# Kernel optimization log

Measured on AMD Instinct MI355X. Metric: run time of the kernel, lower is better.

The kernel has to match this reference:

```python
import jax, jax.numpy as jnp
import numpy as np
from functools import partial

N_QUBIT = 20
K = 1
PAULI_STRINGS = ['IX', 'IY', 'IZ', 'XI', 'XX', 'XY', 'XZ', 'YI', 'YX', 'YY', 'YZ', 'ZI', 'ZX', 'ZY', 'ZZ']

_C = np.float32(np.cos(np.pi / 4))  # = sin(pi/4)
# RY(-pi/2) = [[cos(-pi/4), -sin(-pi/4)], [sin(-pi/4), cos(-pi/4)]]
RY_NEG90 = np.array([[_C, _C], [-_C, _C]], dtype=np.complex64)
# RX(+pi/2) = [[cos(pi/4), -i sin(pi/4)], [-i sin(pi/4), cos(pi/4)]]
RX_POS90 = np.array([[_C, -1j * _C], [-1j * _C, _C]], dtype=np.complex64)


def _rx(t):
    h = t.astype(jnp.complex64) * 0.5
    c, s = jnp.cos(h), jnp.sin(h)
    i = jnp.complex64(1j)
    return jnp.stack([jnp.stack([c, -i * s]), jnp.stack([-i * s, c])])


def _ry(t):
    h = t.astype(jnp.complex64) * 0.5
    c, s = jnp.cos(h), jnp.sin(h)
    return jnp.stack([jnp.stack([c, -s]), jnp.stack([s, c])])


def _rz(t):
    h = t.astype(jnp.complex64) * 0.5
    z = jnp.zeros((), jnp.complex64)
    return jnp.stack([jnp.stack([jnp.exp(-1j * h), z]), jnp.stack([z, jnp.exp(1j * h)])])


def _apply_1q(psi, U, w):
    # psi: flat (2^n,) complex64; apply 2x2 U on wire w (big-endian, wire 0 = MSB)
    psi = psi.reshape(1 << w, 2, -1)
    return jnp.einsum('ab,xby->xay', U, psi).reshape(-1)


def _apply_cnot(psi, q):
    # CNOT with control q, target q+1 (adjacent wires)
    psi = psi.reshape(1 << q, 2, 2, -1)
    return jnp.stack([psi[:, 0], psi[:, 1, ::-1]], axis=1).reshape(-1)


def _two_local(psi, theta, ps, q):
    wires = (q, q + 1)
    if 'I' in ps:
        for p, w in zip(ps, wires):
            if p == 'X':
                psi = _apply_1q(psi, _rx(theta), w)
            elif p == 'Y':
                psi = _apply_1q(psi, _ry(theta), w)
            elif p == 'Z':
                psi = _apply_1q(psi, _rz(theta), w)
    else:
        for p, w in zip(ps, wires):
            if p == 'X':
                psi = _apply_1q(psi, RY_NEG90, w)
            elif p == 'Y':
                psi = _apply_1q(psi, RX_POS90, w)
        psi = _apply_cnot(psi, q)
        psi = _apply_1q(psi, _rz(theta), q + 1)
        psi = _apply_cnot(psi, q)
        for p, w in zip(ps, wires):
            if p == 'X':
                psi = _apply_1q(psi, RY_NEG90, w)
            elif p == 'Y':
                psi = _apply_1q(psi, RX_POS90, w)
    return psi


def _q_block(psi, thetas15, q):
    for i, ps in enumerate(PAULI_STRINGS):
        psi = _two_local(psi, thetas15[i], ps, q)
    return psi


def _circuit(params):
    psi = jnp.zeros(1 << N_QUBIT, jnp.complex64).at[0].set(1.0)
    for layer in range(K):
        for q in range(N_QUBIT - 1):
            # NB: faithful to the source, theta index is i (0..14), NOT q*15+i
            psi = jax.checkpoint(partial(_q_block, q=q))(psi, params[layer, :15])
    return jnp.abs(psi) ** 2


def setup_inputs() -> dict:
    key = jax.random.key(0)
    params = jax.random.normal(key, (K, (N_QUBIT - 1) * 15), dtype=jnp.float32) * np.float32(np.pi / 8)
    return {"params": params}


def reference(params):
    return _circuit(params)
```

## Files before the change

### kernel.cpp

```cpp
#include <hip/hip_runtime.h>

typedef float2 cpx;

__device__ __forceinline__ cpx cmul(cpx a, cpx b){
  return make_float2(a.x*b.x - a.y*b.y, a.x*b.y + a.y*b.x);
}
__device__ __forceinline__ cpx cadd(cpx a, cpx b){ return make_float2(a.x+b.x, a.y+b.y); }
__device__ __forceinline__ cpx czero(){ return make_float2(0.f,0.f); }

__device__ __forceinline__ cpx basis_e(int p, int i, int j){
  const float C = 0.70710678f;
  if (p==1){ float s = (i==1 && j==0) ? -C : C; return make_float2(s, 0.f); }
  else if (p==2){ if (i==j) return make_float2(C,0.f); return make_float2(0.f,-C); }
  else { return make_float2(i==j ? 1.f : 0.f, 0.f); }
}

__device__ __forceinline__ cpx rot_e(int p, int i, int j, float ch, float sh){
  if (p==1){ if (i==j) return make_float2(ch,0.f); return make_float2(0.f,-sh); }
  else if (p==2){ if (i==j) return make_float2(ch,0.f); return make_float2(i==1?sh:-sh, 0.f); }
  else { if (i!=j) return czero(); return make_float2(ch, i==0?-sh:sh); }
}

__device__ __forceinline__ cpx gate_entry(int i, int r, int c, float ch, float sh){
  int pa = i>>2, pb = i&3;
  if (pa==0 || pb==0){
    int p = pa ? pa : pb;
    if (pa) return ((r&1)==(c&1))   ? rot_e(p, r>>1, c>>1, ch, sh) : czero();
    else    return ((r>>1)==(c>>1)) ? rot_e(p, r&1,  c&1,  ch, sh) : czero();
  } else {
    cpx em = make_float2(ch,-sh), ep = make_float2(ch,sh);
    cpx s = czero();
    #pragma unroll
    for (int m=0;m<4;m++){
      cpx Prm = cmul(basis_e(pa, r>>1, m>>1), basis_e(pb, r&1, m&1));
      cpx Pmc = cmul(basis_e(pa, m>>1, c>>1), basis_e(pb, m&1, c&1));
      cpx d = (m==0 || m==3) ? em : ep;
      s = cadd(s, cmul(cmul(Prm, d), Pmc));
    }
    return s;
  }
}

#define SELT(bb, m00,m01,m10,m11) \
  m00 = (bb) ? t100 : t000; m01 = (bb) ? t101 : t001; \
  m10 = (bb) ? t110 : t010; m11 = (bb) ? t111 : t011;

__global__ __launch_bounds__(256) void mps_fused(const float* __restrict__ params,
                                                 float* __restrict__ out){
  __shared__ cpx Gm[16][16];
  __shared__ cpx P[8][16];
  __shared__ cpx Q[4][16];
  __shared__ cpx Tl[8];
  __shared__ cpx u4[16][2];
  __shared__ cpx M4p[16][5];
  __shared__ cpx f4p[16][3];
  const int t = threadIdx.x;

  if (t >= 16){
    int i = t>>4, e = t&15;
    float h = 0.5f*params[i-1];
    Gm[i][e] = gate_entry(i, e>>2, e&3, __cosf(h), __sinf(h));
  }
  __syncthreads();

  if (t < 128){
    int p = t>>4, e = t&15, r = e>>2, c = e&3;
    if (p < 7){
      cpx s = czero();
      #pragma unroll
      for (int k=0;k<4;k++) s = cadd(s, cmul(Gm[2*p+2][r*4+k], Gm[2*p+1][k*4+c]));
      P[p][e] = s;
    } else {
      P[7][e] = Gm[15][e];
    }
  }
  __syncthreads();

  if (t < 64){
    int p = t>>4, e = t&15, r = e>>2, c = e&3;
    cpx s = czero();
    #pragma unroll
    for (int k=0;k<4;k++) s = cadd(s, cmul(P[2*p+1][r*4+k], P[2*p][k*4+c]));
    Q[p][e] = s;
  }
  __syncthreads();

  if (t < 8){
    int z=(t>>2)&1, yi=(t>>1)&1, yo=t&1;
    int a=(z<<1)|yo, b=yi<<1;
    cpx r0=Q[3][a*4+0], r1=Q[3][a*4+1], r2=Q[3][a*4+2], r3=Q[3][a*4+3];
    cpx n0,n1,n2,n3;
    n0 = cadd(cadd(cmul(r0,Q[2][0]), cmul(r1,Q[2][4])), cadd(cmul(r2,Q[2][8]),  cmul(r3,Q[2][12])));
    n1 = cadd(cadd(cmul(r0,Q[2][1]), cmul(r1,Q[2][5])), cadd(cmul(r2,Q[2][9]),  cmul(r3,Q[2][13])));
    n2 = cadd(cadd(cmul(r0,Q[2][2]), cmul(r1,Q[2][6])), cadd(cmul(r2,Q[2][10]), cmul(r3,Q[2][14])));
    n3 = cadd(cadd(cmul(r0,Q[2][3]), cmul(r1,Q[2][7])), cadd(cmul(r2,Q[2][11]), cmul(r3,Q[2][15])));
    r0=n0; r1=n1; r2=n2; r3=n3;
    n0 = cadd(cadd(cmul(r0,Q[1][0]), cmul(r1,Q[1][4])), cadd(cmul(r2,Q[1][8]),  cmul(r3,Q[1][12])));
    n1 = cadd(cadd(cmul(r0,Q[1][1]), cmul(r1,Q[1][5])), cadd(cmul(r2,Q[1][9]),  cmul(r3,Q[1][13])));
    n2 = cadd(cadd(cmul(r0,Q[1][2]), cmul(r1,Q[1][6])), cadd(cmul(r2,Q[1][10]), cmul(r3,Q[1][14])));
    n3 = cadd(cadd(cmul(r0,Q[1][3]), cmul(r1,Q[1][7])), cadd(cmul(r2,Q[1][11]), cmul(r3,Q[1][15])));
    r0=n0; r1=n1; r2=n2; r3=n3;
    cpx s = cadd(cadd(cmul(r0,Q[0][b]), cmul(r1,Q[0][4+b])), cadd(cmul(r2,Q[0][8+b]), cmul(r3,Q[0][12+b])));
    Tl[t] = s;
  }
  __syncthreads();

  if (t < 48){
    cpx t000=Tl[0], t001=Tl[1], t010=Tl[2], t011=Tl[3];
    cpx t100=Tl[4], t101=Tl[5], t110=Tl[6], t111=Tl[7];
    int kind = t>>4, pat = t&15;
    int q3=pat>>3, q2=(pat>>2)&1, q1=(pat>>1)&1, q0=pat&1;
    cpx m00,m01,m10,m11;
    if (kind == 0){
      cpx r0 = q3 ? t100 : t000;
      cpx r1 = q3 ? t101 : t001;
      SELT(q2, m00,m01,m10,m11);
      { cpx n0 = cadd(cmul(r0,m00),cmul(r1,m10)); cpx n1 = cadd(cmul(r0,m01),cmul(r1,m11)); r0=n0; r1=n1; }
      SELT(q1, m00,m01,m10,m11);
      { cpx n0 = cadd(cmul(r0,m00),cmul(r1,m10)); cpx n1 = cadd(cmul(r0,m01),cmul(r1,m11)); r0=n0; r1=n1; }
      SELT(q0, m00,m01,m10,m11);
      { cpx n0 = cadd(cmul(r0,m00),cmul(r1,m10)); cpx n1 = cadd(cmul(r0,m01),cmul(r1,m11)); r0=n0; r1=n1; }
      u4[pat][0]=r0; u4[pat][1]=r1;
    } else if (kind == 1){
      cpx M00,M01,M10,M11;
      SELT(q3, M00,M01,M10,M11);
      SELT(q2, m00,m01,m10,m11);
      { cpx N00=cadd(cmul(M00,m00),cmul(M01,m10)), N01=cadd(cmul(M00,m01),cmul(M01,m11));
        cpx N10=cadd(cmul(M10,m00),cmul(M11,m10)), N11=cadd(cmul(M10,m01),cmul(M11,m11));
        M00=N00; M01=N01; M10=N10; M11=N11; }
      SELT(q1, m00,m01,m10,m11);
      { cpx N00=cadd(cmul(M00,m00),cmul(M01,m10)), N01=cadd(cmul(M00,m01),cmul(M01,m11));
        cpx N10=cadd(cmul(M10,m00),cmul(M11,m10)), N11=cadd(cmul(M10,m01),cmul(M11,m11));
        M00=N00; M01=N01; M10=N10; M11=N11; }
      SELT(q0, m00,m01,m10,m11);
      { cpx N00=cadd(cmul(M00,m00),cmul(M01,m10)), N01=cadd(cmul(M00,m01),cmul(M01,m11));
        cpx N10=cadd(cmul(M10,m00),cmul(M11,m10)), N11=cadd(cmul(M10,m01),cmul(M11,m11));
        M00=N00; M01=N01; M10=N10; M11=N11; }
      M4p[pat][0]=M00; M4p[pat][1]=M01; M4p[pat][2]=M10; M4p[pat][3]=M11;
    } else {
      cpx v0 = q1 ? (q0 ? t101 : t100) : (q0 ? t001 : t000);
      cpx v1 = q1 ? (q0 ? t111 : t110) : (q0 ? t011 : t010);
      SELT(q2, m00,m01,m10,m11);
      { cpx n0 = cadd(cmul(m00,v0),cmul(m01,v1)); cpx n1 = cadd(cmul(m10,v0),cmul(m11,v1)); v0=n0; v1=n1; }
      SELT(q3, m00,m01,m10,m11);
      { cpx n0 = cadd(cmul(m00,v0),cmul(m01,v1)); cpx n1 = cadd(cmul(m10,v0),cmul(m11,v1)); v0=n0; v1=n1; }
      f4p[pat][0]=v0; f4p[pat][1]=v1;
    }
  }
  __syncthreads();

  unsigned bid = blockIdx.x;
  cpx r0 = u4[bid>>6][0], r1 = u4[bid>>6][1];
  {
    const cpx* Ma = M4p[(bid>>2)&15u];
    cpx n0 = cadd(cmul(r0,Ma[0]), cmul(r1,Ma[2]));
    cpx n1 = cadd(cmul(r0,Ma[1]), cmul(r1,Ma[3]));
    r0=n0; r1=n1;
  }
  {
    const cpx* Mb = M4p[((bid&3u)<<2)|((unsigned)(t>>6)&3u)];
    cpx n0 = cadd(cmul(r0,Mb[0]), cmul(r1,Mb[2]));
    cpx n1 = cadd(cmul(r0,Mb[1]), cmul(r1,Mb[3]));
    r0=n0; r1=n1;
  }
  {
    const cpx* Mc = M4p[(t>>2)&15];
    cpx n0 = cadd(cmul(r0,Mc[0]), cmul(r1,Mc[2]));
    cpx n1 = cadd(cmul(r0,Mc[1]), cmul(r1,Mc[3]));
    r0=n0; r1=n1;
  }
  int fb = (t&3)<<2;
  float4 res; cpx y;
  y = cadd(cmul(r0, f4p[fb  ][0]), cmul(r1, f4p[fb  ][1])); res.x = y.x*y.x + y.y*y.y;
  y = cadd(cmul(r0, f4p[fb|1][0]), cmul(r1, f4p[fb|1][1])); res.y = y.x*y.x + y.y*y.y;
  y = cadd(cmul(r0, f4p[fb|2][0]), cmul(r1, f4p[fb|2][1])); res.z = y.x*y.x + y.y*y.y;
  y = cadd(cmul(r0, f4p[fb|3][0]), cmul(r1, f4p[fb|3][1])); res.w = y.x*y.x + y.y*y.y;
  ((float4*)out)[(bid<<8) | (unsigned)t] = res;
}

extern "C" void kernel_launch(void* const* d_in, const int* in_sizes, int n_in,
                              void* d_out, int out_size, void* d_ws, size_t ws_size,
                              hipStream_t stream) {
  const float* params = (const float*)d_in[0];
  mps_fused<<<1024, 256, 0, stream>>>(params, (float*)d_out);
}
```

Baseline: 11.57 us.

## Run gate-product tree in one wavefront with wave barriers and closed-form gates

Moves the 4x4 gate-matrix product reduction (P, Q, new R level, Tl) and the transfer-matrix setup into a single 64-thread wavefront, replacing block-wide __syncthreads with wave-level barriers plus an LDS waitcnt. Adds a tree-reduction level so the serial chain of matrix products in the Tl stage becomes one short product. Also replaces the basis-sum construction of the two-qubit Pauli rotation gate with a closed form cos*P + i*sin*diag entry. The aim is to shorten the serial prologue that every block repeats before writing its outputs. It relies on the LDS accesses being ordered within the wave by the wave barrier and waitcnt.

```diff
diff --git a/kernel.cpp b/kernel.cpp
--- a/kernel.cpp
+++ b/kernel.cpp
@@ -8,17 +8,17 @@
 __device__ __forceinline__ cpx cadd(cpx a, cpx b){ return make_float2(a.x+b.x, a.y+b.y); }
 __device__ __forceinline__ cpx czero(){ return make_float2(0.f,0.f); }
 
-__device__ __forceinline__ cpx basis_e(int p, int i, int j){
-  const float C = 0.70710678f;
-  if (p==1){ float s = (i==1 && j==0) ? -C : C; return make_float2(s, 0.f); }
-  else if (p==2){ if (i==j) return make_float2(C,0.f); return make_float2(0.f,-C); }
-  else { return make_float2(i==j ? 1.f : 0.f, 0.f); }
-}
-
 __device__ __forceinline__ cpx rot_e(int p, int i, int j, float ch, float sh){
   if (p==1){ if (i==j) return make_float2(ch,0.f); return make_float2(0.f,-sh); }
   else if (p==2){ if (i==j) return make_float2(ch,0.f); return make_float2(i==1?sh:-sh, 0.f); }
   else { if (i!=j) return czero(); return make_float2(ch, i==0?-sh:sh); }
+}
+
+__device__ __forceinline__ cpx Ae(int p, int i, int j){
+  if (p==3) return make_float2(i==j?1.f:0.f, 0.f);
+  if (i==j) return czero();
+  if (p==1) return make_float2(i==0?1.f:-1.f, 0.f);
+  return make_float2(0.f,-1.f);
 }
 
 __device__ __forceinline__ cpx gate_entry(int i, int r, int c, float ch, float sh){
@@ -27,19 +27,16 @@
     int p = pa ? pa : pb;
     if (pa) return ((r&1)==(c&1))   ? rot_e(p, r>>1, c>>1, ch, sh) : czero();
     else    return ((r>>1)==(c>>1)) ? rot_e(p, r&1,  c&1,  ch, sh) : czero();
-  } else {
-    cpx em = make_float2(ch,-sh), ep = make_float2(ch,sh);
-    cpx s = czero();
-    #pragma unroll
-    for (int m=0;m<4;m++){
-      cpx Prm = cmul(basis_e(pa, r>>1, m>>1), basis_e(pb, r&1, m&1));
-      cpx Pmc = cmul(basis_e(pa, m>>1, c>>1), basis_e(pb, m&1, c&1));
-      cpx d = (m==0 || m==3) ? em : ep;
-      s = cadd(s, cmul(cmul(Prm, d), Pmc));
-    }
-    return s;
   }
+  cpx a = cmul(Ae(pa, r>>1, c>>1), Ae(pb, r&1, c&1));
+  cpx g = make_float2(ch*a.x, ch*a.y);
+  if (r==c){ float zz = (r==0 || r==3) ? 1.f : -1.f; g.y -= sh*zz; }
+  return g;
 }
+
+#define WSYNC() do { __builtin_amdgcn_wave_barrier(); \
+  asm volatile("s_waitcnt lgkmcnt(0)" ::: "memory"); \
+  __builtin_amdgcn_wave_barrier(); } while(0)
 
 #define SELT(bb, m00,m01,m10,m11) \
   m00 = (bb) ? t100 : t000; m01 = (bb) ? t101 : t001; \
@@ -50,6 +47,7 @@
   __shared__ cpx Gm[16][16];
   __shared__ cpx P[8][16];
   __shared__ cpx Q[4][16];
+  __shared__ cpx R[2][16];
   __shared__ cpx Tl[8];
   __shared__ cpx u4[16][2];
   __shared__ cpx M4p[16][5];
@@ -63,88 +61,91 @@
   }
   __syncthreads();
 
-  if (t < 128){
-    int p = t>>4, e = t&15, r = e>>2, c = e&3;
-    if (p < 7){
+  if (t < 64){
+    #pragma unroll
+    for (int jj=0; jj<2; ++jj){
+      int j = t + jj*64;
+      int p = j>>4, e = j&15, r = e>>2, c = e&3;
+      if (p < 7){
+        cpx s = czero();
+        #pragma unroll
+        for (int k=0;k<4;k++) s = cadd(s, cmul(Gm[2*p+2][r*4+k], Gm[2*p+1][k*4+c]));
+        P[p][e] = s;
+      } else {
+        P[7][e] = Gm[15][e];
+      }
+    }
+    WSYNC();
+
+    {
+      int p = t>>4, e = t&15, r = e>>2, c = e&3;
       cpx s = czero();
       #pragma unroll
-      for (int k=0;k<4;k++) s = cadd(s, cmul(Gm[2*p+2][r*4+k], Gm[2*p+1][k*4+c]));
-      P[p][e] = s;
-    } else {
-      P[7][e] = Gm[15][e];
+      for (int k=0;k<4;k++) s = cadd(s, cmul(P[2*p+1][r*4+k], P[2*p][k*4+c]));
+      Q[p][e] = s;
     }
-  }
-  __syncthreads();
+    WSYNC();
 
-  if (t < 64){
-    int p = t>>4, e = t&15, r = e>>2, c = e&3;
-    cpx s = czero();
-    #pragma unroll
-    for (int k=0;k<4;k++) s = cadd(s, cmul(P[2*p+1][r*4+k], P[2*p][k*4+c]));
-    Q[p][e] = s;
-  }
-  __syncthreads();
+    if (t < 32){
+      int p = t>>4, e = t&15, r = e>>2, c = e&3;
+      cpx s = czero();
+      #pragma unroll
+      for (int k=0;k<4;k++) s = cadd(s, cmul(Q[2*p+1][r*4+k], Q[2*p][k*4+c]));
+      R[p][e] = s;
+    }
+    WSYNC();
 
-  if (t < 8){
-    int z=(t>>2)&1, yi=(t>>1)&1, yo=t&1;
-    int a=(z<<1)|yo, b=yi<<1;
-    cpx r0=Q[3][a*4+0], r1=Q[3][a*4+1], r2=Q[3][a*4+2], r3=Q[3][a*4+3];
-    cpx n0,n1,n2,n3;
-    n0 = cadd(cadd(cmul(r0,Q[2][0]), cmul(r1,Q[2][4])), cadd(cmul(r2,Q[2][8]),  cmul(r3,Q[2][12])));
-    n1 = cadd(cadd(cmul(r0,Q[2][1]), cmul(r1,Q[2][5])), cadd(cmul(r2,Q[2][9]),  cmul(r3,Q[2][13])));
-    n2 = cadd(cadd(cmul(r0,Q[2][2]), cmul(r1,Q[2][6])), cadd(cmul(r2,Q[2][10]), cmul(r3,Q[2][14])));
-    n3 = cadd(cadd(cmul(r0,Q[2][3]), cmul(r1,Q[2][7])), cadd(cmul(r2,Q[2][11]), cmul(r3,Q[2][15])));
-    r0=n0; r1=n1; r2=n2; r3=n3;
-    n0 = cadd(cadd(cmul(r0,Q[1][0]), cmul(r1,Q[1][4])), cadd(cmul(r2,Q[1][8]),  cmul(r3,Q[1][12])));
-    n1 = cadd(cadd(cmul(r0,Q[1][1]), cmul(r1,Q[1][5])), cadd(cmul(r2,Q[1][9]),  cmul(r3,Q[1][13])));
-    n2 = cadd(cadd(cmul(r0,Q[1][2]), cmul(r1,Q[1][6])), cadd(cmul(r2,Q[1][10]), cmul(r3,Q[1][14])));
-    n3 = cadd(cadd(cmul(r0,Q[1][3]), cmul(r1,Q[1][7])), cadd(cmul(r2,Q[1][11]), cmul(r3,Q[1][15])));
-    r0=n0; r1=n1; r2=n2; r3=n3;
-    cpx s = cadd(cadd(cmul(r0,Q[0][b]), cmul(r1,Q[0][4+b])), cadd(cmul(r2,Q[0][8+b]), cmul(r3,Q[0][12+b])));
-    Tl[t] = s;
-  }
-  __syncthreads();
+    if (t < 8){
+      int z=(t>>2)&1, yi=(t>>1)&1, yo=t&1;
+      int a=(z<<1)|yo, b=yi<<1;
+      cpx s = czero();
+      #pragma unroll
+      for (int k=0;k<4;k++) s = cadd(s, cmul(R[1][a*4+k], R[0][k*4+b]));
+      Tl[t] = s;
+    }
+    WSYNC();
 
-  if (t < 48){
-    cpx t000=Tl[0], t001=Tl[1], t010=Tl[2], t011=Tl[3];
-    cpx t100=Tl[4], t101=Tl[5], t110=Tl[6], t111=Tl[7];
-    int kind = t>>4, pat = t&15;
-    int q3=pat>>3, q2=(pat>>2)&1, q1=(pat>>1)&1, q0=pat&1;
-    cpx m00,m01,m10,m11;
-    if (kind == 0){
-      cpx r0 = q3 ? t100 : t000;
-      cpx r1 = q3 ? t101 : t001;
-      SELT(q2, m00,m01,m10,m11);
-      { cpx n0 = cadd(cmul(r0,m00),cmul(r1,m10)); cpx n1 = cadd(cmul(r0,m01),cmul(r1,m11)); r0=n0; r1=n1; }
-      SELT(q1, m00,m01,m10,m11);
-      { cpx n0 = cadd(cmul(r0,m00),cmul(r1,m10)); cpx n1 = cadd(cmul(r0,m01),cmul(r1,m11)); r0=n0; r1=n1; }
-      SELT(q0, m00,m01,m10,m11);
-      { cpx n0 = cadd(cmul(r0,m00),cmul(r1,m10)); cpx n1 = cadd(cmul(r0,m01),cmul(r1,m11)); r0=n0; r1=n1; }
-      u4[pat][0]=r0; u4[pat][1]=r1;
-    } else if (kind == 1){
-      cpx M00,M01,M10,M11;
-      SELT(q3, M00,M01,M10,M11);
-      SELT(q2, m00,m01,m10,m11);
-      { cpx N00=cadd(cmul(M00,m00),cmul(M01,m10)), N01=cadd(cmul(M00,m01),cmul(M01,m11));
-        cpx N10=cadd(cmul(M10,m00),cmul(M11,m10)), N11=cadd(cmul(M10,m01),cmul(M11,m11));
-        M00=N00; M01=N01; M10=N10; M11=N11; }
-      SELT(q1, m00,m01,m10,m11);
-      { cpx N00=cadd(cmul(M00,m00),cmul(M01,m10)), N01=cadd(cmul(M00,m01),cmul(M01,m11));
-        cpx N10=cadd(cmul(M10,m00),cmul(M11,m10)), N11=cadd(cmul(M10,m01),cmul(M11,m11));
-        M00=N00; M01=N01; M10=N10; M11=N11; }
-      SELT(q0, m00,m01,m10,m11);
-      { cpx N00=cadd(cmul(M00,m00),cmul(M01,m10)), N01=cadd(cmul(M00,m01),cmul(M01,m11));
-        cpx N10=cadd(cmul(M10,m00),cmul(M11,m10)), N11=cadd(cmul(M10,m01),cmul(M11,m11));
-        M00=N00; M01=N01; M10=N10; M11=N11; }
-      M4p[pat][0]=M00; M4p[pat][1]=M01; M4p[pat][2]=M10; M4p[pat][3]=M11;
-    } else {
-      cpx v0 = q1 ? (q0 ? t101 : t100) : (q0 ? t001 : t000);
-      cpx v1 = q1 ? (q0 ? t111 : t110) : (q0 ? t011 : t010);
-      SELT(q2, m00,m01,m10,m11);
-      { cpx n0 = cadd(cmul(m00,v0),cmul(m01,v1)); cpx n1 = cadd(cmul(m10,v0),cmul(m11,v1)); v0=n0; v1=n1; }
-      SELT(q3, m00,m01,m10,m11);
-      { cpx n0 = cadd(cmul(m00,v0),cmul(m01,v1)); cpx n1 = cadd(cmul(m10,v0),cmul(m11,v1)); v0=n0; v1=n1; }
-      f4p[pat][0]=v0; f4p[pat][1]=v1;
+    if (t < 48){
+      cpx t000=Tl[0], t001=Tl[1], t010=Tl[2], t011=Tl[3];
+      cpx t100=Tl[4], t101=Tl[5], t110=Tl[6], t111=Tl[7];
+      int kind = t>>4, pat = t&15;
+      int q3=pat>>3, q2=(pat>>2)&1, q1=(pat>>1)&1, q0=pat&1;
+      cpx m00,m01,m10,m11;
+      if (kind == 0){
+        cpx r0 = q3 ? t100 : t000;
+        cpx r1 = q3 ? t101 : t001;
+        SELT(q2, m00,m01,m10,m11);
+        { cpx n0 = cadd(cmul(r0,m00),cmul(r1,m10)); cpx n1 = cadd(cmul(r0,m01),cmul(r1,m11)); r0=n0; r1=n1; }
+        SELT(q1, m00,m01,m10,m11);
+        { cpx n0 = cadd(cmul(r0,m00),cmul(r1,m10)); cpx n1 = cadd(cmul(r0,m01),cmul(r1,m11)); r0=n0; r1=n1; }
+        SELT(q0, m00,m01,m10,m11);
+        { cpx n0 = cadd(cmul(r0,m00),cmul(r1,m10)); cpx n1 = cadd(cmul(r0,m01),cmul(r1,m11)); r0=n0; r1=n1; }
+        u4[pat][0]=r0; u4[pat][1]=r1;
+      } else if (kind == 1){
+        cpx M00,M01,M10,M11;
+        SELT(q3, M00,M01,M10,M11);
+        SELT(q2, m00,m01,m10,m11);
+        { cpx N00=cadd(cmul(M00,m00),cmul(M01,m10)), N01=cadd(cmul(M00,m01),cmul(M01,m11));
+          cpx N10=cadd(cmul(M10,m00),cmul(M11,m10)), N11=cadd(cmul(M10,m01),cmul(M11,m11));
+          M00=N00; M01=N01; M10=N10; M11=N11; }
+        SELT(q1, m00,m01,m10,m11);
+        { cpx N00=cadd(cmul(M00,m00),cmul(M01,m10)), N01=cadd(cmul(M00,m01),cmul(M01,m11));
+          cpx N10=cadd(cmul(M10,m00),cmul(M11,m10)), N11=cadd(cmul(M10,m01),cmul(M11,m11));
+          M00=N00; M01=N01; M10=N10; M11=N11; }
+        SELT(q0, m00,m01,m10,m11);
+        { cpx N00=cadd(cmul(M00,m00),cmul(M01,m10)), N01=cadd(cmul(M00,m01),cmul(M01,m11));
+          cpx N10=cadd(cmul(M10,m00),cmul(M11,m10)), N11=cadd(cmul(M10,m01),cmul(M11,m11));
+          M00=N00; M01=N01; M10=N10; M11=N11; }
+        M4p[pat][0]=M00; M4p[pat][1]=M01; M4p[pat][2]=M10; M4p[pat][3]=M11;
+      } else {
+        cpx v0 = q1 ? (q0 ? t101 : t100) : (q0 ? t001 : t000);
+        cpx v1 = q1 ? (q0 ? t111 : t110) : (q0 ? t011 : t010);
+        SELT(q2, m00,m01,m10,m11);
+        { cpx n0 = cadd(cmul(m00,v0),cmul(m01,v1)); cpx n1 = cadd(cmul(m10,v0),cmul(m11,v1)); v0=n0; v1=n1; }
+        SELT(q3, m00,m01,m10,m11);
+        { cpx n0 = cadd(cmul(m00,v0),cmul(m01,v1)); cpx n1 = cadd(cmul(m10,v0),cmul(m11,v1)); v0=n0; v1=n1; }
+        f4p[pat][0]=v0; f4p[pat][1]=v1;
+      }
     }
   }
   __syncthreads();
```

Result: faster. 10.89 us, median of 2 (-5.9%).
